# Kernel optimization log

Hardware: AMD Instinct MI355X
Metric: run time of the kernel (lower is better)

Reference implementation:

```python
import jax, jax.numpy as jnp
import numpy as np

SNAPPING_GAIN = 30.0


def setup_inputs() -> dict:
    key = jax.random.key(0)
    k1, k2 = jax.random.split(key)
    latent_coeffs = jax.random.normal(k1, (16, 2048, 1024), dtype=jnp.float32)
    # NMF basis is non-negative; 1024 atoms of dim 900 (30x30 ARC grids)
    basis_vectors = jax.random.uniform(k2, (1024, 900), dtype=jnp.float32)
    return {"latent_coeffs": latent_coeffs, "basis_vectors": basis_vectors}


def reference(latent_coeffs, basis_vectors):
    # [B, K, C] -> sharpened softmax over codes
    probs = jax.nn.softmax(latent_coeffs * SNAPPING_GAIN, axis=-1)
    indices = jnp.argmax(probs, axis=-1)                        # [B, K] int
    one_hot = jax.nn.one_hot(indices, probs.shape[-1], dtype=probs.dtype)
    # straight-through: value == one_hot, gradient flows through probs
    one_hot_st = probs + jax.lax.stop_gradient(one_hot - probs)
    # [B,K,C] @ [C,D] -> [B,K,D] (effectively a row-gather of the basis)
    quantized = jnp.einsum('bkc,cd->bkd', one_hot_st, basis_vectors)
    return quantized, indices
```

## Files before the change

kernel.cpp:

```cpp
#include <hip/hip_runtime.h>


#define C_DIM 1024
#define D_DIM 900

__global__ __launch_bounds__(256) void basisvq_kernel(
    const float* __restrict__ latent,
    const float* __restrict__ basis,
    float* __restrict__ out_q,
    float* __restrict__ out_idx)
{
    const int row = blockIdx.x;
    const int tid = threadIdx.x;

    const float4* lrow = reinterpret_cast<const float4*>(latent + (size_t)row * C_DIM);
    float4 v = lrow[tid];
    float m = v.x;
    int mi  = tid * 4;
    if (v.y > m) { m = v.y; mi = tid * 4 + 1; }
    if (v.z > m) { m = v.z; mi = tid * 4 + 2; }
    if (v.w > m) { m = v.w; mi = tid * 4 + 3; }

    #pragma unroll
    for (int off = 32; off > 0; off >>= 1) {
        float om = __shfl_down(m, off, 64);
        int   oi = __shfl_down(mi, off, 64);
        if (om > m || (om == m && oi < mi)) { m = om; mi = oi; }
    }

    __shared__ float sm[4];
    __shared__ int   si[4];
    __shared__ int   bidx;
    const int lane = tid & 63;
    const int wid  = tid >> 6;
    if (lane == 0) { sm[wid] = m; si[wid] = mi; }
    __syncthreads();
    if (tid == 0) {
        float bm = sm[0]; int bi = si[0];
        #pragma unroll
        for (int w = 1; w < 4; ++w) {
            if (sm[w] > bm || (sm[w] == bm && si[w] < bi)) { bm = sm[w]; bi = si[w]; }
        }
        bidx = bi;
        out_idx[row] = (float)bi;
    }
    __syncthreads();
    const int idx = bidx;

    const float4* b4 = reinterpret_cast<const float4*>(basis + (size_t)idx * D_DIM);
    float4*       o4 = reinterpret_cast<float4*>(out_q + (size_t)row * D_DIM);
    if (tid < 225) o4[tid] = b4[tid];
}

extern "C" void kernel_launch(void* const* d_in, const int* in_sizes, int n_in,
                              void* d_out, int out_size, void* d_ws, size_t ws_size,
                              hipStream_t stream) {
    const float* latent = (const float*)d_in[0];
    const float* basis  = (const float*)d_in[1];
    (void)n_in; (void)d_ws; (void)ws_size;

    const int rows = in_sizes[0] / C_DIM;
    float* out_q   = (float*)d_out;
    float* out_idx = (float*)d_out + (size_t)rows * D_DIM;
    (void)out_size;

    basisvq_kernel<<<rows, 256, 0, stream>>>(latent, basis, out_q, out_idx);
}
```

Before: 54.71 us.

## Process one row per wavefront with nontemporal loads and stores

Each wavefront now owns a whole row. It loads four float4 chunks per lane and does the argmax entirely with wave shuffles, so the shared-memory cross-wave reduction and both block barriers are gone. The latent reads and quantized-output writes use nontemporal hints to avoid polluting the cache, while the basis gather keeps normal loads so it stays cached. The kernel is memory-bound, so any gain depends on better latency hiding and cache behavior rather than less traffic.

```diff
diff --git a/kernel.cpp b/kernel.cpp
--- a/kernel.cpp
+++ b/kernel.cpp
@@ -4,52 +4,67 @@
 #define C_DIM 1024
 #define D_DIM 900
 
+typedef float vfloat4 __attribute__((ext_vector_type(4)));
+
 __global__ __launch_bounds__(256) void basisvq_kernel(
     const float* __restrict__ latent,
     const float* __restrict__ basis,
     float* __restrict__ out_q,
-    float* __restrict__ out_idx)
+    float* __restrict__ out_idx,
+    int rows)
 {
-    const int row = blockIdx.x;
-    const int tid = threadIdx.x;
+    const int lane = threadIdx.x & 63;
+    const int wid  = threadIdx.x >> 6;
+    const int row  = blockIdx.x * 4 + wid;
+    if (row >= rows) return;
 
-    const float4* lrow = reinterpret_cast<const float4*>(latent + (size_t)row * C_DIM);
-    float4 v = lrow[tid];
-    float m = v.x;
-    int mi  = tid * 4;
-    if (v.y > m) { m = v.y; mi = tid * 4 + 1; }
-    if (v.z > m) { m = v.z; mi = tid * 4 + 2; }
-    if (v.w > m) { m = v.w; mi = tid * 4 + 3; }
+    const vfloat4* lrow = reinterpret_cast<const vfloat4*>(latent + (size_t)row * C_DIM);
+    vfloat4 v0 = __builtin_nontemporal_load(&lrow[lane]);
+    vfloat4 v1 = __builtin_nontemporal_load(&lrow[lane + 64]);
+    vfloat4 v2 = __builtin_nontemporal_load(&lrow[lane + 128]);
+    vfloat4 v3 = __builtin_nontemporal_load(&lrow[lane + 192]);
+
+    float m = v0[0];
+    int   mi = lane * 4;
+    #pragma unroll
+    for (int e = 1; e < 4; ++e)
+        if (v0[e] > m) { m = v0[e]; mi = lane * 4 + e; }
+    #pragma unroll
+    for (int e = 0; e < 4; ++e) {
+        int c = (64 + lane) * 4 + e;
+        if (v1[e] > m) { m = v1[e]; mi = c; }
+    }
+    #pragma unroll
+    for (int e = 0; e < 4; ++e) {
+        int c = (128 + lane) * 4 + e;
+        if (v2[e] > m) { m = v2[e]; mi = c; }
+    }
+    #pragma unroll
+    for (int e = 0; e < 4; ++e) {
+        int c = (192 + lane) * 4 + e;
+        if (v3[e] > m) { m = v3[e]; mi = c; }
+    }
 
     #pragma unroll
     for (int off = 32; off > 0; off >>= 1) {
-        float om = __shfl_down(m, off, 64);
-        int   oi = __shfl_down(mi, off, 64);
+        float om = __shfl_xor(m, off, 64);
+        int   oi = __shfl_xor(mi, off, 64);
         if (om > m || (om == m && oi < mi)) { m = om; mi = oi; }
     }
+    const int idx = mi;
 
-    __shared__ float sm[4];
-    __shared__ int   si[4];
-    __shared__ int   bidx;
-    const int lane = tid & 63;
-    const int wid  = tid >> 6;
-    if (lane == 0) { sm[wid] = m; si[wid] = mi; }
-    __syncthreads();
-    if (tid == 0) {
-        float bm = sm[0]; int bi = si[0];
-        #pragma unroll
-        for (int w = 1; w < 4; ++w) {
-            if (sm[w] > bm || (sm[w] == bm && si[w] < bi)) { bm = sm[w]; bi = si[w]; }
+    if (lane == 0) out_idx[row] = (float)idx;
+
+    const vfloat4* b4 = reinterpret_cast<const vfloat4*>(basis + (size_t)idx * D_DIM);
+    vfloat4*       o4 = reinterpret_cast<vfloat4*>(out_q + (size_t)row * D_DIM);
+    #pragma unroll
+    for (int j = 0; j < 4; ++j) {
+        int t = 64 * j + lane;
+        if (t < 225) {
+            vfloat4 bv = b4[t];
+            __builtin_nontemporal_store(bv, &o4[t]);
         }
-        bidx = bi;
-        out_idx[row] = (float)bi;
     }
-    __syncthreads();
-    const int idx = bidx;
-
-    const float4* b4 = reinterpret_cast<const float4*>(basis + (size_t)idx * D_DIM);
-    float4*       o4 = reinterpret_cast<float4*>(out_q + (size_t)row * D_DIM);
-    if (tid < 225) o4[tid] = b4[tid];
 }
 
 extern "C" void kernel_launch(void* const* d_in, const int* in_sizes, int n_in,
@@ -57,12 +72,12 @@
                               hipStream_t stream) {
     const float* latent = (const float*)d_in[0];
     const float* basis  = (const float*)d_in[1];
-    (void)n_in; (void)d_ws; (void)ws_size;
+    (void)n_in; (void)d_ws; (void)ws_size; (void)out_size;
 
     const int rows = in_sizes[0] / C_DIM;
     float* out_q   = (float*)d_out;
     float* out_idx = (float*)d_out + (size_t)rows * D_DIM;
-    (void)out_size;
 
-    basisvq_kernel<<<rows, 256, 0, stream>>>(latent, basis, out_q, out_idx);
+    const int blocks = (rows + 3) / 4;
+    basisvq_kernel<<<blocks, 256, 0, stream>>>(latent, basis, out_q, out_idx, rows);
 }
```

After: 50.51 us. 7.7% less time.
